# Kernel optimization log

Measured on AMD Instinct MI355X. Metric: run time of the kernel, lower is better.

Reference implementation:

```python
import jax, jax.numpy as jnp
import numpy as np

B, LQ, LK, DQ, DK, DV = 8, 2048, 2048, 1024, 1024, 1024
TOP_K = 64
NEG_INF = float('-inf')


def setup_inputs() -> dict:
    key = jax.random.key(0)
    kq, kk, kv, km, kw = jax.random.split(key, 5)
    queries = jax.random.normal(kq, (B, LQ, DQ), dtype=jnp.float32)
    keys = jax.random.normal(kk, (B, LK, DK), dtype=jnp.float32)
    values = jax.random.normal(kv, (B, LK, DV), dtype=jnp.float32)
    mask = jax.random.randint(km, (B, LQ, LK), 0, 2, dtype=jnp.int32)
    # nn.Linear(query_dim, key_dim, bias=False) weight: [key_dim, query_dim]
    W = jax.random.normal(kw, (DK, DQ), dtype=jnp.float32) / np.sqrt(DQ)
    return {"queries": queries, "keys": keys, "values": values,
            "mask": mask, "W": W, "top_k": TOP_K}


def reference(queries, keys, values, mask, W, top_k):
    # scores = (queries @ W.T) @ keys^T  -> [B, LQ, LK]  (method='general')
    q_proj = jnp.einsum('bqd,kd->bqk', queries, W)  # [B, LQ, DK]
    scores = jnp.einsum('bqd,btd->bqt', q_proj, keys)  # [B, LQ, LK]
    scores = jnp.where(mask == 0, NEG_INF, scores)
    alphas = jax.nn.softmax(scores, axis=-1)
    alphas = jnp.where(jnp.isnan(alphas), 0.0, alphas)  # fully-masked rows -> 0
    # top-k: zero out non-top-k probabilities, then re-softmax over the
    # resulting tensor (zeros contribute exp(0)=1, matching torch semantics)
    _, idx = jax.lax.top_k(alphas, top_k)  # [B, LQ, top_k]
    b_idx = jnp.arange(alphas.shape[0])[:, None, None]
    q_idx = jnp.arange(alphas.shape[1])[None, :, None]
    topk_mask = jnp.zeros(alphas.shape, alphas.dtype).at[b_idx, q_idx, idx].set(1.0)
    alphas = jnp.where(topk_mask == 0, 0.0, alphas)
    alphas = jax.nn.softmax(alphas, axis=-1)
    alphas = jnp.where(jnp.isnan(alphas), 0.0, alphas)
    # dropout_rate = 0.0 -> identity
    return jnp.einsum('bqt,btd->bqd', alphas, values)  # [B, LQ, DV]
```

## Files before the change

kernel.cpp:

```cpp
#include <hip/hip_runtime.h>
#include <math.h>

#define BATCH 8
#define SEQ   2048
#define DIM   1024
#define TOPK  64
#define NEGMASK -1e30f
#define CAND_THRESH 16.0f
#define CAP 28

typedef _Float16 f16;
typedef _Float16 f16x8 __attribute__((ext_vector_type(8)));
typedef float f32x4 __attribute__((ext_vector_type(4)));

__device__ __forceinline__ void async_load16(const void* g, void* l) {
  __builtin_amdgcn_global_load_lds(
      (const __attribute__((address_space(1))) void*)g,
      (__attribute__((address_space(3))) void*)l, 16, 0, 0);
}

__device__ __forceinline__ uint2 cvt4(float4 v) {
  union { f16 h[4]; uint2 u; } pk;
  pk.h[0] = (f16)v.x; pk.h[1] = (f16)v.y; pk.h[2] = (f16)v.z; pk.h[3] = (f16)v.w;
  return pk.u;
}

__global__ __launch_bounds__(256) void prep_kernel(
    const float* __restrict__ queries, const float* __restrict__ keys,
    const float* __restrict__ W,
    const int4* __restrict__ mask4, const float* __restrict__ values,
    f16* __restrict__ q16, f16* __restrict__ k16, f16* __restrict__ w16,
    unsigned long long* __restrict__ mb, float* __restrict__ partial) {
  const int blk = blockIdx.x;
  if (blk < 8192) {
    const float4* src = (const float4*)(blk < 4096 ? queries : keys);
    uint2* dst = (uint2*)(blk < 4096 ? q16 : k16);
    const int base = (blk & 4095) * 1024 + threadIdx.x;
    float4 v0 = src[base];
    float4 v1 = src[base + 256];
    float4 v2 = src[base + 512];
    float4 v3 = src[base + 768];
    dst[base]       = cvt4(v0);
    dst[base + 256] = cvt4(v1);
    dst[base + 512] = cvt4(v2);
    dst[base + 768] = cvt4(v3);
  } else if (blk < 8448) {
    const float4* src = (const float4*)W;
    uint2* dst = (uint2*)w16;
    const int base = (blk - 8192) * 1024 + threadIdx.x;
    float4 v0 = src[base];
    float4 v1 = src[base + 256];
    float4 v2 = src[base + 512];
    float4 v3 = src[base + 768];
    dst[base]       = cvt4(v0);
    dst[base + 256] = cvt4(v1);
    dst[base + 512] = cvt4(v2);
    dst[base + 768] = cvt4(v3);
  } else if (blk < 10496) {
    const int bid = blk - 8448;
    const int wave = threadIdx.x >> 6, lane = threadIdx.x & 63;
    const size_t nGrp = (size_t)16384 * 8;
    for (size_t g = (size_t)bid * 16 + wave * 4; g < nGrp; g += 2048 * 16) {
      int4 v0 = mask4[(g + 0) * 64 + lane];
      int4 v1 = mask4[(g + 1) * 64 + lane];
      int4 v2 = mask4[(g + 2) * 64 + lane];
      int4 v3 = mask4[(g + 3) * 64 + lane];
      unsigned long long a0 = __ballot(v0.x != 0);
      unsigned long long a1 = __ballot(v0.y != 0);
      unsigned long long a2 = __ballot(v0.z != 0);
      unsigned long long a3 = __ballot(v0.w != 0);
      unsigned long long b0 = __ballot(v1.x != 0);
      unsigned long long b1 = __ballot(v1.y != 0);
      unsigned long long b2 = __ballot(v1.z != 0);
      unsigned long long b3 = __ballot(v1.w != 0);
      unsigned long long c0 = __ballot(v2.x != 0);
      unsigned long long c1 = __ballot(v2.y != 0);
      unsigned long long c2 = __ballot(v2.z != 0);
      unsigned long long c3 = __ballot(v2.w != 0);
      unsigned long long d0 = __ballot(v3.x != 0);
      unsigned long long d1 = __ballot(v3.y != 0);
      unsigned long long d2 = __ballot(v3.z != 0);
      unsigned long long d3 = __ballot(v3.w != 0);
      if (lane == 0) {
        mb[g * 4 + 0]  = a0; mb[g * 4 + 1]  = a1;
        mb[g * 4 + 2]  = a2; mb[g * 4 + 3]  = a3;
        mb[g * 4 + 4]  = b0; mb[g * 4 + 5]  = b1;
        mb[g * 4 + 6]  = b2; mb[g * 4 + 7]  = b3;
        mb[g * 4 + 8]  = c0; mb[g * 4 + 9]  = c1;
        mb[g * 4 + 10] = c2; mb[g * 4 + 11] = c3;
        mb[g * 4 + 12] = d0; mb[g * 4 + 13] = d1;
        mb[g * 4 + 14] = d2; mb[g * 4 + 15] = d3;
      }
    }
  } else {
    const int bid = blk - 10496;
    int tc = bid >> 5;
    int b  = (bid >> 2) & 7;
    int dg = bid & 3;
    int d  = dg * 256 + threadIdx.x;
    const float* vp = values + ((size_t)b * SEQ + (size_t)tc * 64) * DIM + d;
    float s = 0.f;
    #pragma unroll 8
    for (int t = 0; t < 64; ++t) s += vp[(size_t)t * DIM];
    partial[((size_t)tc * BATCH + b) * DIM + d] = s;
  }
}


#define STAGEK(KOFF, BUF)                                                   \
  async_load16(srcA0 + (KOFF), smA + (BUF) * 8192 + wave * 2048);           \
  async_load16(srcA1 + (KOFF), smA + (BUF) * 8192 + wave * 2048 + 1024);    \
  async_load16(srcB0 + (KOFF), smB + (BUF) * 8192 + wave * 2048);           \
  async_load16(srcB1 + (KOFF), smB + (BUF) * 8192 + wave * 2048 + 1024);

#define GEMM_PROLOGUE(APTR, BPTR)                                           \
  const int tid = threadIdx.x;                                              \
  const int wave = tid >> 6, lane = tid & 63;                               \
  const int wm = (wave >> 1) * 64, wn = (wave & 1) * 64;                    \
  const int r0 = wave * 32 + (lane >> 2);                                   \
  const int c16 = (lane & 3) ^ ((r0 >> 1) & 3);                            \
  const f16* srcA0 = (APTR) + (size_t)(m0 + r0) * DIM + c16 * 8;           \
  const f16* srcA1 = (APTR) + (size_t)(m0 + r0 + 16) * DIM + c16 * 8;      \
  const f16* srcB0 = (BPTR) + (size_t)(n0 + r0) * DIM + c16 * 8;           \
  const f16* srcB1 = (BPTR) + (size_t)(n0 + r0 + 16) * DIM + c16 * 8;      \
  int offA[4], offB[4];                                                     \
  _Pragma("unroll")                                                         \
  for (int i = 0; i < 4; ++i) {                                             \
    int r = wm + i * 16 + (lane & 15);                                      \
    offA[i] = r * 64 + ((lane >> 4) ^ ((r >> 1) & 3)) * 16;                 \
    int rn = wn + i * 16 + (lane & 15);                                     \
    offB[i] = rn * 64 + ((lane >> 4) ^ ((rn >> 1) & 3)) * 16;               \
  }                                                                         \
  f32x4 acc[4][4];                                                          \
  _Pragma("unroll")                                                         \
  for (int i = 0; i < 4; ++i)                                               \
    _Pragma("unroll")                                                       \
    for (int j = 0; j < 4; ++j)                                             \
      acc[i][j] = (f32x4){0.f, 0.f, 0.f, 0.f};                              \
  STAGEK(0, 0)                                                              \
  int cur = 0;                                                              \
  for (int k0 = 0; k0 < DIM; k0 += 32) {                                    \
    const int nxt = cur ^ 1;                                                \
    if (k0 + 32 < DIM) {                                                    \
      STAGEK(k0 + 32, nxt)                                                  \
      asm volatile("s_waitcnt vmcnt(4)" ::: "memory");                      \
    } else {                                                                \
      asm volatile("s_waitcnt vmcnt(0)" ::: "memory");                      \
    }                                                                       \
    __builtin_amdgcn_s_barrier();                                           \
    asm volatile("" ::: "memory");                                          \
    f16x8 af[4], bf[4];                                                     \
    _Pragma("unroll")                                                       \
    for (int i = 0; i < 4; ++i) {                                           \
      af[i] = *(const f16x8*)(smA + cur * 8192 + offA[i]);                  \
      bf[i] = *(const f16x8*)(smB + cur * 8192 + offB[i]);                  \
    }                                                                       \
    _Pragma("unroll")                                                       \
    for (int i = 0; i < 4; ++i)                                             \
      _Pragma("unroll")                                                     \
      for (int j = 0; j < 4; ++j)                                           \
        acc[i][j] = __builtin_amdgcn_mfma_f32_16x16x32_f16(                 \
            af[i], bf[j], acc[i][j], 0, 0, 0);                              \
    asm volatile("" ::: "memory");                                          \
    __builtin_amdgcn_s_barrier();                                           \
    cur = nxt;                                                              \
  }

__global__ __launch_bounds__(256, 3) void gemm_qproj(
    const f16* __restrict__ A, const f16* __restrict__ Bw,
    f16* __restrict__ C,
    const float* __restrict__ partial, float* __restrict__ colsum) {
  __shared__ __align__(128) char smA[16384];
  __shared__ __align__(128) char smB[16384];
  if (blockIdx.x >= 1024) {
    int idx = ((int)blockIdx.x - 1024) * 256 + threadIdx.x;
    float s = 0.f;
    #pragma unroll
    for (int tc = 0; tc < 32; ++tc) s += partial[(size_t)tc * 8192 + idx];
    colsum[idx] = s;
    return;
  }
  const int swz = ((int)blockIdx.x & 7) * 128 + ((int)blockIdx.x >> 3);
  const int m0 = (swz >> 3) * 128;
  const int n0 = (swz & 7) * 128;
  GEMM_PROLOGUE(A, Bw)
  const int cr = m0 + wm + (lane >> 4) * 4;
  const int cc = n0 + wn + (lane & 15);
  #pragma unroll
  for (int i = 0; i < 4; ++i)
    #pragma unroll
    for (int j = 0; j < 4; ++j)
      #pragma unroll
      for (int reg = 0; reg < 4; ++reg)
        C[(size_t)(cr + i * 16 + reg) * DIM + cc + j * 16] = (f16)acc[i][j][reg];
}

__global__ __launch_bounds__(256, 3) void gemm_scores(
    const f16* __restrict__ QP, const f16* __restrict__ K16,
    const unsigned long long* __restrict__ maskbits,
    float2* __restrict__ cand,
    int* __restrict__ counts) {
  __shared__ __align__(128) char smA[16384];
  __shared__ __align__(128) char smB[16384];
  const int swz = ((int)blockIdx.x & 7) * 256 + ((int)blockIdx.x >> 3);
  const int m0 = (swz >> 4) * 128;
  const int n0 = (swz & 15) * 128;
  const int b  = m0 >> 11;
  const f16* Bk = K16 + (size_t)b * SEQ * DIM;
  GEMM_PROLOGUE(QP, Bk)

  const int g  = lane >> 4;
  const int lc = lane & 15;

  const int grp = (n0 + wn) >> 8;
  const int basebit = ((n0 + wn) & 255) >> 2;
  #pragma unroll
  for (int i = 0; i < 4; ++i)
    #pragma unroll
    for (int reg = 0; reg < 4; ++reg) {
      const int r = wm + i * 16 + g * 4 + reg;
      const unsigned long long mw =
          maskbits[(size_t)(m0 + r) * 32 + grp * 4 + (lc & 3)];
      #pragma unroll
      for (int j = 0; j < 4; ++j)
        if (!((mw >> (basebit + j * 4 + (lc >> 2))) & 1ull))
          acc[i][j][reg] = NEGMASK;
    }

  float* hm = (float*)smA;
  #pragma unroll
  for (int i = 0; i < 4; ++i)
    #pragma unroll
    for (int reg = 0; reg < 4; ++reg) {
      const int r = wm + i * 16 + g * 4 + reg;
      float m4 = fmaxf(fmaxf(acc[i][0][reg], acc[i][1][reg]),
                       fmaxf(acc[i][2][reg], acc[i][3][reg]));
      #pragma unroll
      for (int off = 8; off >= 1; off >>= 1) m4 = fmaxf(m4, __shfl_xor(m4, off));
      if (lc == 0) hm[r * 2 + (wn >> 6)] = m4;
    }
  __syncthreads();

  const int pairbase = (n0 >> 7) * 2 + (wn >> 6);
  #pragma unroll
  for (int i = 0; i < 4; ++i)
    #pragma unroll
    for (int reg = 0; reg < 4; ++reg) {
      const int r = wm + i * 16 + g * 4 + reg;
      const float tm = fmaxf(hm[r * 2], hm[r * 2 + 1]);
      const float thresh = fmaxf(tm - CAND_THRESH, -1e29f);
      float2* slot = cand + ((size_t)(m0 + r) * 32 + pairbase) * CAP;
      int cnt = 0;
      #pragma unroll
      for (int j = 0; j < 4; ++j) {
        const float s = acc[i][j][reg];
        const bool c = s > thresh;
        const unsigned long long bal = __ballot(c);
        const int seg = (int)((bal >> (g * 16)) & 0xFFFFull);
        const int pos = cnt + __popc(seg & ((1 << lc) - 1));
        if (c && pos < CAP) {
          float2 e; e.x = s; e.y = __int_as_float(n0 + wn + j * 16 + lc);
          slot[pos] = e;
        }
        cnt += __popc(seg);
      }
      if (lc == 0) counts[(size_t)(m0 + r) * 32 + pairbase] = cnt < CAP ? cnt : CAP;
    }
}

__global__ __launch_bounds__(512) void topk_kernel(
    const float2* __restrict__ cand,
    const int*    __restrict__ counts,
    const float*  __restrict__ values,
    const float*  __restrict__ colsum,
    float* __restrict__ out)
{
  __shared__ float ssc[8][128];
  __shared__ int   sidx[8][128];
  const int wave = threadIdx.x >> 6;
  const int lane = threadIdx.x & 63;
  const int grow = blockIdx.x * 8 + wave;
  const int b    = grow >> 11;
  float* msc = ssc[wave];
  int*   mix = sidx[wave];

  int cnt_p = 0;
  if (lane < 32) cnt_p = counts[(size_t)grow * 32 + lane];
  const float2* myslots = cand + ((size_t)grow * 32 + lane) * CAP;

  float mv = -3e38f;
  for (int k = 0; k < cnt_p; ++k) mv = fmaxf(mv, myslots[k].x);
  #pragma unroll
  for (int off = 32; off > 0; off >>= 1) mv = fmaxf(mv, __shfl_xor(mv, off));
  const bool dead = (mv <= -1e29f);

  float total_g = 0.f;
  f32x4 oacc[4];
  #pragma unroll
  for (int j = 0; j < 4; ++j) oacc[j] = (f32x4){0.f, 0.f, 0.f, 0.f};
  const float* vbase = values + (size_t)b * SEQ * DIM;

  if (!dead) {
    const float thresh = mv - CAND_THRESH;
    int f = 0; float zp = 0.f;
    for (int k = 0; k < cnt_p; ++k) {
      float s = myslots[k].x;
      if (s > thresh) { ++f; zp += __expf(s - mv); }
    }
    int incl = f;
    #pragma unroll
    for (int off = 1; off < 64; off <<= 1) {
      int t = __shfl_up(incl, off);
      if (lane >= off) incl += t;
    }
    const int base = incl - f;
    const int F = __shfl(incl, 63);
    #pragma unroll
    for (int off = 32; off > 0; off >>= 1) zp += __shfl_xor(zp, off);
    const float Z = zp;
    int w = 0;
    for (int k = 0; k < cnt_p; ++k) {
      float2 cv = myslots[k];
      if (cv.x > thresh) {
        int p = base + w;
        if (p < 128) { msc[p] = cv.x; mix[p] = __float_as_int(cv.y); }
        ++w;
      }
    }
    asm volatile("s_waitcnt lgkmcnt(0)" ::: "memory");

    if (F <= TOPK) {
      for (int c = 0; c < F; ++c) {
        float g = expm1f(__expf(msc[c] - mv) / Z);
        total_g += g;
        const float* vrow = vbase + (size_t)mix[c] * DIM;
        #pragma unroll
        for (int j = 0; j < 4; ++j) {
          f32x4 v = *(const f32x4*)(vrow + j * 256 + lane * 4);
          #pragma unroll
          for (int e = 0; e < 4; ++e) oacc[j][e] = fmaf(g, v[e], oacc[j][e]);
        }
      }
    } else {
      const int nlist = F < 128 ? F : 128;
      for (int itk = 0; itk < TOPK; ++itk) {
        float bv = -3e38f; int bi = 1 << 30; int bsl = -1;
        #pragma unroll
        for (int h = 0; h < 2; ++h) {
          int sl = lane + h * 64;
          if (sl < nlist) {
            float v = msc[sl]; int id = mix[sl];
            if (v > bv || (v == bv && id < bi)) { bv = v; bi = id; bsl = sl; }
          }
        }
        #pragma unroll
        for (int off = 32; off > 0; off >>= 1) {
          float ov = __shfl_xor(bv, off);
          int   oi = __shfl_xor(bi, off);
          int   os = __shfl_xor(bsl, off);
          if (ov > bv || (ov == bv && oi < bi)) { bv = ov; bi = oi; bsl = os; }
        }
        if (bv <= -1e29f) break;
        float g = expm1f(__expf(bv - mv) / Z);
        total_g += g;
        const float* vrow = vbase + (size_t)bi * DIM;
        #pragma unroll
        for (int j = 0; j < 4; ++j) {
          f32x4 v = *(const f32x4*)(vrow + j * 256 + lane * 4);
          #pragma unroll
          for (int e = 0; e < 4; ++e) oacc[j][e] = fmaf(g, v[e], oacc[j][e]);
        }
        if (lane == 0) msc[bsl] = -3e38f;
        asm volatile("s_waitcnt lgkmcnt(0)" ::: "memory");
      }
    }
  }

  const float inv = 1.0f / (2048.0f + total_g);
  const float* cs = colsum + (size_t)b * DIM;
  float* orow = out + (size_t)grow * DIM;
  #pragma unroll
  for (int j = 0; j < 4; ++j) {
    f32x4 c = *(const f32x4*)(cs + j * 256 + lane * 4);
    f32x4 o;
    #pragma unroll
    for (int e = 0; e < 4; ++e) o[e] = (c[e] + oacc[j][e]) * inv;
    *(f32x4*)(orow + j * 256 + lane * 4) = o;
  }
}

extern "C" void kernel_launch(void* const* d_in, const int* in_sizes, int n_in,
                              void* d_out, int out_size, void* d_ws, size_t ws_size,
                              hipStream_t stream) {
  const float* queries = (const float*)d_in[0];
  const float* keys    = (const float*)d_in[1];
  const float* values  = (const float*)d_in[2];
  const int*   mask    = (const int*)d_in[3];
  const float* W       = (const float*)d_in[4];
  float* out = (float*)d_out;

  char* base = (char*)d_ws;
  float2* cand   = (float2*)base;
  f16*   q16     = (f16*)base;
  f16*   w16     = (f16*)(base + (size_t)32 * 1024 * 1024);
  int*   counts  = (int*)(base + (size_t)112 * 1024 * 1024);
  unsigned long long* maskbits =
      (unsigned long long*)(base + (size_t)114 * 1024 * 1024);
  float* colsum  = (float*)(base + (size_t)118 * 1024 * 1024);
  float* partial = (float*)(base + (size_t)119 * 1024 * 1024);
  f16*   qp16    = (f16*)(base + (size_t)128 * 1024 * 1024);
  f16*   k16     = (f16*)(base + (size_t)160 * 1024 * 1024);

  prep_kernel<<<11520, 256, 0, stream>>>(queries, keys, W, (const int4*)mask,
                                         values, q16, k16, w16, maskbits,
                                         partial);
  gemm_qproj<<<1056, 256, 0, stream>>>(q16, w16, qp16, partial, colsum);
  gemm_scores<<<2048, 256, 0, stream>>>(qp16, k16, maskbits, cand, counts);
  topk_kernel<<<2048, 512, 0, stream>>>(cand, counts, values, colsum, out);
}
```

Before: 296.7 us.

## Redistribute prep work across kernels and read raw mask in score epilogue

Removes the mask bit-packing pass and reads the int32 mask directly in the scores GEMM epilogue. The key conversion and value partial column sums move into the q-projection launch, and the colsum reduction moves into the scores launch. The aim is to shrink the standalone prep kernel and let memory-bound work overlap with GEMM blocks. In exchange, the epilogue now reads 4-byte mask elements per score instead of packed bits, so that step moves more bytes.

```diff
diff --git a/kernel.cpp b/kernel.cpp
--- a/kernel.cpp
+++ b/kernel.cpp
@@ -26,16 +26,13 @@
 }
 
 __global__ __launch_bounds__(256) void prep_kernel(
-    const float* __restrict__ queries, const float* __restrict__ keys,
-    const float* __restrict__ W,
-    const int4* __restrict__ mask4, const float* __restrict__ values,
-    f16* __restrict__ q16, f16* __restrict__ k16, f16* __restrict__ w16,
-    unsigned long long* __restrict__ mb, float* __restrict__ partial) {
+    const float* __restrict__ queries, const float* __restrict__ W,
+    f16* __restrict__ q16, f16* __restrict__ w16) {
   const int blk = blockIdx.x;
-  if (blk < 8192) {
-    const float4* src = (const float4*)(blk < 4096 ? queries : keys);
-    uint2* dst = (uint2*)(blk < 4096 ? q16 : k16);
-    const int base = (blk & 4095) * 1024 + threadIdx.x;
+  if (blk < 4096) {
+    const float4* src = (const float4*)queries;
+    uint2* dst = (uint2*)q16;
+    const int base = blk * 1024 + threadIdx.x;
     float4 v0 = src[base];
     float4 v1 = src[base + 256];
     float4 v2 = src[base + 512];
@@ -44,10 +41,10 @@
     dst[base + 256] = cvt4(v1);
     dst[base + 512] = cvt4(v2);
     dst[base + 768] = cvt4(v3);
-  } else if (blk < 8448) {
+  } else {
     const float4* src = (const float4*)W;
     uint2* dst = (uint2*)w16;
-    const int base = (blk - 8192) * 1024 + threadIdx.x;
+    const int base = (blk - 4096) * 1024 + threadIdx.x;
     float4 v0 = src[base];
     float4 v1 = src[base + 256];
     float4 v2 = src[base + 512];
@@ -56,53 +53,6 @@
     dst[base + 256] = cvt4(v1);
     dst[base + 512] = cvt4(v2);
     dst[base + 768] = cvt4(v3);
-  } else if (blk < 10496) {
-    const int bid = blk - 8448;
-    const int wave = threadIdx.x >> 6, lane = threadIdx.x & 63;
-    const size_t nGrp = (size_t)16384 * 8;
-    for (size_t g = (size_t)bid * 16 + wave * 4; g < nGrp; g += 2048 * 16) {
-      int4 v0 = mask4[(g + 0) * 64 + lane];
-      int4 v1 = mask4[(g + 1) * 64 + lane];
-      int4 v2 = mask4[(g + 2) * 64 + lane];
-      int4 v3 = mask4[(g + 3) * 64 + lane];
-      unsigned long long a0 = __ballot(v0.x != 0);
-      unsigned long long a1 = __ballot(v0.y != 0);
-      unsigned long long a2 = __ballot(v0.z != 0);
-      unsigned long long a3 = __ballot(v0.w != 0);
-      unsigned long long b0 = __ballot(v1.x != 0);
-      unsigned long long b1 = __ballot(v1.y != 0);
-      unsigned long long b2 = __ballot(v1.z != 0);
-      unsigned long long b3 = __ballot(v1.w != 0);
-      unsigned long long c0 = __ballot(v2.x != 0);
-      unsigned long long c1 = __ballot(v2.y != 0);
-      unsigned long long c2 = __ballot(v2.z != 0);
-      unsigned long long c3 = __ballot(v2.w != 0);
-      unsigned long long d0 = __ballot(v3.x != 0);
-      unsigned long long d1 = __ballot(v3.y != 0);
-      unsigned long long d2 = __ballot(v3.z != 0);
-      unsigned long long d3 = __ballot(v3.w != 0);
-      if (lane == 0) {
-        mb[g * 4 + 0]  = a0; mb[g * 4 + 1]  = a1;
-        mb[g * 4 + 2]  = a2; mb[g * 4 + 3]  = a3;
-        mb[g * 4 + 4]  = b0; mb[g * 4 + 5]  = b1;
-        mb[g * 4 + 6]  = b2; mb[g * 4 + 7]  = b3;
-        mb[g * 4 + 8]  = c0; mb[g * 4 + 9]  = c1;
-        mb[g * 4 + 10] = c2; mb[g * 4 + 11] = c3;
-        mb[g * 4 + 12] = d0; mb[g * 4 + 13] = d1;
-        mb[g * 4 + 14] = d2; mb[g * 4 + 15] = d3;
-      }
-    }
-  } else {
-    const int bid = blk - 10496;
-    int tc = bid >> 5;
-    int b  = (bid >> 2) & 7;
-    int dg = bid & 3;
-    int d  = dg * 256 + threadIdx.x;
-    const float* vp = values + ((size_t)b * SEQ + (size_t)tc * 64) * DIM + d;
-    float s = 0.f;
-    #pragma unroll 8
-    for (int t = 0; t < 64; ++t) s += vp[(size_t)t * DIM];
-    partial[((size_t)tc * BATCH + b) * DIM + d] = s;
   }
 }
 
@@ -169,15 +119,35 @@
 __global__ __launch_bounds__(256, 3) void gemm_qproj(
     const f16* __restrict__ A, const f16* __restrict__ Bw,
     f16* __restrict__ C,
-    const float* __restrict__ partial, float* __restrict__ colsum) {
+    const float* __restrict__ keys, f16* __restrict__ k16,
+    const float* __restrict__ values, float* __restrict__ partial) {
   __shared__ __align__(128) char smA[16384];
   __shared__ __align__(128) char smB[16384];
+  if (blockIdx.x >= 5120) {
+    const int bid = (int)blockIdx.x - 5120;
+    int tc = bid >> 5;
+    int b  = (bid >> 2) & 7;
+    int dg = bid & 3;
+    int d  = dg * 256 + threadIdx.x;
+    const float* vp = values + ((size_t)b * SEQ + (size_t)tc * 64) * DIM + d;
+    float s = 0.f;
+    #pragma unroll 8
+    for (int t = 0; t < 64; ++t) s += vp[(size_t)t * DIM];
+    partial[((size_t)tc * BATCH + b) * DIM + d] = s;
+    return;
+  }
   if (blockIdx.x >= 1024) {
-    int idx = ((int)blockIdx.x - 1024) * 256 + threadIdx.x;
-    float s = 0.f;
-    #pragma unroll
-    for (int tc = 0; tc < 32; ++tc) s += partial[(size_t)tc * 8192 + idx];
-    colsum[idx] = s;
+    const float4* src = (const float4*)keys;
+    uint2* dst = (uint2*)k16;
+    const int base = ((int)blockIdx.x - 1024) * 1024 + threadIdx.x;
+    float4 v0 = src[base];
+    float4 v1 = src[base + 256];
+    float4 v2 = src[base + 512];
+    float4 v3 = src[base + 768];
+    dst[base]       = cvt4(v0);
+    dst[base + 256] = cvt4(v1);
+    dst[base + 512] = cvt4(v2);
+    dst[base + 768] = cvt4(v3);
     return;
   }
   const int swz = ((int)blockIdx.x & 7) * 128 + ((int)blockIdx.x >> 3);
@@ -197,11 +167,20 @@
 
 __global__ __launch_bounds__(256, 3) void gemm_scores(
     const f16* __restrict__ QP, const f16* __restrict__ K16,
-    const unsigned long long* __restrict__ maskbits,
+    const int* __restrict__ mask,
     float2* __restrict__ cand,
-    int* __restrict__ counts) {
+    int* __restrict__ counts,
+    const float* __restrict__ partial, float* __restrict__ colsum) {
   __shared__ __align__(128) char smA[16384];
   __shared__ __align__(128) char smB[16384];
+  if (blockIdx.x >= 2048) {
+    int idx = ((int)blockIdx.x - 2048) * 256 + threadIdx.x;
+    float s = 0.f;
+    #pragma unroll
+    for (int tc = 0; tc < 32; ++tc) s += partial[(size_t)tc * 8192 + idx];
+    colsum[idx] = s;
+    return;
+  }
   const int swz = ((int)blockIdx.x & 7) * 256 + ((int)blockIdx.x >> 3);
   const int m0 = (swz >> 4) * 128;
   const int n0 = (swz & 15) * 128;
@@ -212,19 +191,17 @@
   const int g  = lane >> 4;
   const int lc = lane & 15;
 
-  const int grp = (n0 + wn) >> 8;
-  const int basebit = ((n0 + wn) & 255) >> 2;
   #pragma unroll
   for (int i = 0; i < 4; ++i)
     #pragma unroll
     for (int reg = 0; reg < 4; ++reg) {
       const int r = wm + i * 16 + g * 4 + reg;
-      const unsigned long long mw =
-          maskbits[(size_t)(m0 + r) * 32 + grp * 4 + (lc & 3)];
-      #pragma unroll
-      for (int j = 0; j < 4; ++j)
-        if (!((mw >> (basebit + j * 4 + (lc >> 2))) & 1ull))
-          acc[i][j][reg] = NEGMASK;
+      const int* mp = mask + (size_t)(m0 + r) * SEQ + n0 + wn + lc;
+      int m0v = mp[0], m1v = mp[16], m2v = mp[32], m3v = mp[48];
+      if (m0v == 0) acc[i][0][reg] = NEGMASK;
+      if (m1v == 0) acc[i][1][reg] = NEGMASK;
+      if (m2v == 0) acc[i][2][reg] = NEGMASK;
+      if (m3v == 0) acc[i][3][reg] = NEGMASK;
     }
 
   float* hm = (float*)smA;
@@ -404,17 +381,14 @@
   f16*   q16     = (f16*)base;
   f16*   w16     = (f16*)(base + (size_t)32 * 1024 * 1024);
   int*   counts  = (int*)(base + (size_t)112 * 1024 * 1024);
-  unsigned long long* maskbits =
-      (unsigned long long*)(base + (size_t)114 * 1024 * 1024);
   float* colsum  = (float*)(base + (size_t)118 * 1024 * 1024);
   float* partial = (float*)(base + (size_t)119 * 1024 * 1024);
   f16*   qp16    = (f16*)(base + (size_t)128 * 1024 * 1024);
   f16*   k16     = (f16*)(base + (size_t)160 * 1024 * 1024);
 
-  prep_kernel<<<11520, 256, 0, stream>>>(queries, keys, W, (const int4*)mask,
-                                         values, q16, k16, w16, maskbits,
-                                         partial);
-  gemm_qproj<<<1056, 256, 0, stream>>>(q16, w16, qp16, partial, colsum);
-  gemm_scores<<<2048, 256, 0, stream>>>(qp16, k16, maskbits, cand, counts);
+  prep_kernel<<<4352, 256, 0, stream>>>(queries, W, q16, w16);
+  gemm_qproj<<<6144, 256, 0, stream>>>(q16, w16, qp16, keys, k16, values, partial);
+  gemm_scores<<<2080, 256, 0, stream>>>(qp16, k16, mask, cand, counts,
+                                        partial, colsum);
   topk_kernel<<<2048, 512, 0, stream>>>(cand, counts, values, colsum, out);
 }
```

Measured after the change: 275.5 us. -7.2%, faster.
